# Kernel optimization log

Measured on AMD Instinct MI355X. Metric: run time of the kernel, lower is better.

The kernel has to match this reference:

```python
import jax, jax.numpy as jnp
import numpy as np

NUM_NODES = 100000
NUM_REL = 8
HIDDEN = 128
NUM_EDGES = 1600000
NUM_LAYERS = 2


def setup_inputs() -> dict:
    key = jax.random.key(0)
    k1, k2, k3, k4, k5 = jax.random.split(key, 5)
    x = jnp.arange(NUM_NODES, dtype=jnp.int64)
    edge_index = jax.random.randint(k1, (2, NUM_EDGES), 0, NUM_NODES, dtype=jnp.int64)
    edge_type = jax.random.randint(k2, (NUM_EDGES,), 0, NUM_REL, dtype=jnp.int64)
    emb = jax.random.normal(k3, (NUM_NODES, HIDDEN), dtype=jnp.float32) * 0.1
    W = jax.random.normal(k4, (NUM_LAYERS, NUM_REL, HIDDEN, HIDDEN), dtype=jnp.float32) * (1.0 / np.sqrt(HIDDEN))
    root = jax.random.normal(k5, (NUM_LAYERS, HIDDEN, HIDDEN), dtype=jnp.float32) * (1.0 / np.sqrt(HIDDEN))
    bias = jnp.zeros((NUM_LAYERS, HIDDEN), dtype=jnp.float32)
    return {"x": x, "edge_index": edge_index, "edge_type": edge_type,
            "emb": emb, "W": W, "root": root, "bias": bias}


def _rgcn_conv(h, src, dst, etype, W_l, root_l, bias_l):
    # h: [N, d]; W_l: [R, d, d]
    n = h.shape[0]
    r = W_l.shape[0]
    # Transform all nodes by every relation weight: [R, N, d]
    xW = jnp.einsum('nd,rdf->rnf', h, W_l)
    # Per-edge message gathered by (relation, source): [E, d]
    msg = xW[etype, src]
    # Mean-normalize per (target node, relation), matching PyG aggr='mean'
    seg = dst * r + etype  # combined (node, relation) segment id
    cnt = jax.ops.segment_sum(jnp.ones(msg.shape[0], dtype=h.dtype), seg,
                              num_segments=n * r)
    norm = 1.0 / jnp.maximum(cnt[seg], 1.0)
    agg = jax.ops.segment_sum(msg * norm[:, None], dst, num_segments=n)
    return agg + h @ root_l + bias_l


def reference(x, edge_index, edge_type, emb, W, root, bias):
    src, dst = edge_index[0], edge_index[1]
    h = emb[x]  # embedding lookup
    for l in range(NUM_LAYERS):
        h = _rgcn_conv(h, src, dst, edge_type, W[l], root[l], bias[l])
        h = jax.nn.relu(h)
    return h
```

## Files before the change

kernel.cpp:

```cpp
#include <hip/hip_runtime.h>

typedef unsigned int u32;
typedef unsigned short u16;
typedef __attribute__((ext_vector_type(8))) short short8;
typedef __attribute__((ext_vector_type(4))) float f32x4;

#define DD 128
#define RREL 8
#define NKT 9
#define SCAN_CHUNK 4096

static __device__ __forceinline__ u16 f2bf(float f) {
  u32 u = __builtin_bit_cast(u32, f);
  u32 r = (u + 0x7fffu + ((u >> 16) & 1u)) >> 16;
  return (u16)r;
}
static __device__ __forceinline__ float bflo(u32 v) { return __builtin_bit_cast(float, v << 16); }
static __device__ __forceinline__ float bfhi(u32 v) { return __builtin_bit_cast(float, v & 0xffff0000u); }

__global__ __launch_bounds__(256) void k_convw(const float* __restrict__ W,
                                               const float* __restrict__ root,
                                               uint4* __restrict__ wt) {
  int t = blockIdx.x * 256 + threadIdx.x;
  if (t >= 2 * NKT * 2048) return;
  int l = t / (NKT * 2048);
  int rem = t - l * (NKT * 2048);
  int kt = rem >> 11;
  int pos = rem & 2047;
  int col = pos >> 4;
  int cbx = pos & 15;
  int cb = cbx ^ (col & 7);
  int k0 = kt * DD + cb * 8;
  u16 vals[8];
#pragma unroll
  for (int i = 0; i < 8; ++i) {
    int k = k0 + i;
    float v;
    if (k < DD) {
      v = root[(size_t)l * DD * DD + k * DD + col];
    } else {
      int km = k - DD;
      v = W[((size_t)l * RREL + (km >> 7)) * DD * DD + (size_t)(km & 127) * DD + col];
    }
    vals[i] = f2bf(v);
  }
  wt[t] = *(uint4*)vals;
}

__global__ __launch_bounds__(256) void k_gather(const int* __restrict__ x,
                                                const float* __restrict__ emb,
                                                u16* __restrict__ h0, int N) {
  int t = blockIdx.x * 256 + threadIdx.x;
  if (t >= N * 16) return;
  int node = t >> 4, part = t & 15;
  const float4* e4 = (const float4*)(emb + (size_t)x[node] * DD + part * 8);
  float4 f0 = e4[0], f1 = e4[1];
  uint4 u;
  u.x = (u32)f2bf(f0.x) | ((u32)f2bf(f0.y) << 16);
  u.y = (u32)f2bf(f0.z) | ((u32)f2bf(f0.w) << 16);
  u.z = (u32)f2bf(f1.x) | ((u32)f2bf(f1.y) << 16);
  u.w = (u32)f2bf(f1.z) | ((u32)f2bf(f1.w) << 16);
  *(uint4*)(h0 + (size_t)node * DD + part * 8) = u;
}

__global__ __launch_bounds__(256) void k_hist(const int* __restrict__ ei,
                                              const int* __restrict__ et,
                                              int* __restrict__ cnt, int E) {
  int base = (blockIdx.x * 256 + threadIdx.x) * 4;
  if (base + 3 < E) {
    int4 d4 = *(const int4*)(ei + E + base);
    int4 t4 = *(const int4*)(et + base);
    atomicAdd(&cnt[d4.x * 8 + t4.x], 1);
    atomicAdd(&cnt[d4.y * 8 + t4.y], 1);
    atomicAdd(&cnt[d4.z * 8 + t4.z], 1);
    atomicAdd(&cnt[d4.w * 8 + t4.w], 1);
  } else {
    for (int e = base; e < E; ++e) atomicAdd(&cnt[ei[E + e] * 8 + et[e]], 1);
  }
}

__global__ __launch_bounds__(256) void k_scan_reduce(const int* __restrict__ cnt,
                                                     int* __restrict__ blksum, int nseg) {
  __shared__ int s[256];
  int b = blockIdx.x, t = threadIdx.x;
  int base = b * SCAN_CHUNK;
  int sum = 0;
  for (int i = 0; i < 16; ++i) {
    int idx = base + i * 256 + t;
    if (idx < nseg) sum += cnt[idx];
  }
  s[t] = sum;
  __syncthreads();
  for (int st = 128; st > 0; st >>= 1) {
    if (t < st) s[t] += s[t + st];
    __syncthreads();
  }
  if (t == 0) blksum[b] = s[0];
}

__global__ void k_scan_top(int* __restrict__ blksum, int nblk, int* __restrict__ off,
                           int nseg, int E) {
  if (threadIdx.x == 0 && blockIdx.x == 0) {
    int run = 0;
    for (int b = 0; b < nblk; ++b) { int v = blksum[b]; blksum[b] = run; run += v; }
    off[nseg] = E;
  }
}

__global__ __launch_bounds__(256) void k_scan_write(const int* __restrict__ cnt,
                                                    const int* __restrict__ blksum,
                                                    int* __restrict__ off, int nseg) {
  __shared__ int s[256];
  int b = blockIdx.x, t = threadIdx.x;
  int base = b * SCAN_CHUNK + t * 16;
  int v[16];
  int sum = 0;
#pragma unroll
  for (int i = 0; i < 16; ++i) {
    int idx = base + i;
    v[i] = (idx < nseg) ? cnt[idx] : 0;
    sum += v[i];
  }
  s[t] = sum;
  __syncthreads();
  for (int st = 1; st < 256; st <<= 1) {
    int add = (t >= st) ? s[t - st] : 0;
    __syncthreads();
    s[t] += add;
    __syncthreads();
  }
  int run = blksum[b] + s[t] - sum;
#pragma unroll
  for (int i = 0; i < 16; ++i) {
    int idx = base + i;
    if (idx < nseg) off[idx] = run;
    run += v[i];
  }
}

__global__ __launch_bounds__(256) void k_scatter(const int* __restrict__ ei,
                                                 const int* __restrict__ et,
                                                 int* __restrict__ fill,
                                                 int* __restrict__ sorted, int E) {
  int base = (blockIdx.x * 256 + threadIdx.x) * 4;
  if (base + 3 < E) {
    int4 s4 = *(const int4*)(ei + base);
    int4 d4 = *(const int4*)(ei + E + base);
    int4 t4 = *(const int4*)(et + base);
    int p0 = atomicAdd(&fill[d4.x * 8 + t4.x], 1);
    int p1 = atomicAdd(&fill[d4.y * 8 + t4.y], 1);
    int p2 = atomicAdd(&fill[d4.z * 8 + t4.z], 1);
    int p3 = atomicAdd(&fill[d4.w * 8 + t4.w], 1);
    sorted[p0] = s4.x;
    sorted[p1] = s4.y;
    sorted[p2] = s4.z;
    sorted[p3] = s4.w;
  } else {
    for (int e = base; e < E; ++e) {
      int pos = atomicAdd(&fill[ei[E + e] * 8 + et[e]], 1);
      sorted[pos] = ei[e];
    }
  }
}

static __device__ __forceinline__ void add8(float* a, uint4 v) {
  a[0] += bflo(v.x); a[1] += bfhi(v.x);
  a[2] += bflo(v.y); a[3] += bfhi(v.y);
  a[4] += bflo(v.z); a[5] += bfhi(v.z);
  a[6] += bflo(v.w); a[7] += bfhi(v.w);
}

template <bool LAST>
__global__ __launch_bounds__(512, 4) void k_fused(const u16* __restrict__ hin,
                                                  const int* __restrict__ off,
                                                  const int* __restrict__ sorted,
                                                  const uint4* __restrict__ wt,
                                                  const float* __restrict__ bias,
                                                  u16* __restrict__ hout,
                                                  float* __restrict__ dout, int M) {
  __shared__ uint4 ldsB[2][2048];
  int tid = threadIdx.x, wave = tid >> 6, lane = tid & 63;
  int p = lane & 15, q = lane >> 4;
  int row = blockIdx.x * 128 + wave * 16 + p;
  int arc = row < M ? row : M - 1;
  f32x4 acc[8];
#pragma unroll
  for (int c = 0; c < 8; ++c) acc[c] = (f32x4)0.f;

#define STAGE(KT, BUF)                                                                   \
  do {                                                                                   \
    const uint4* gsrc = wt + (size_t)(KT) * 2048;                                        \
    _Pragma("unroll") for (int i_ = 0; i_ < 4; ++i_) {                                   \
      int cid_ = i_ * 512 + tid;                                                         \
      __builtin_amdgcn_global_load_lds(                                                  \
          (const __attribute__((address_space(1))) uint4*)(gsrc + cid_),                 \
          (__attribute__((address_space(3))) uint4*)&ldsB[BUF][cid_], 16, 0, 0);         \
    }                                                                                    \
  } while (0)

  STAGE(0, 0);
  for (int kt = 0; kt < NKT; ++kt) {
    short8 afrag[4];
    if (kt == 0) {
      const short8* ap = (const short8*)(hin + (size_t)arc * DD) + q;
#pragma unroll
      for (int kc = 0; kc < 4; ++kc) afrag[kc] = ap[kc * 4];
    } else {
      int r = kt - 1;
      int s = 0, e = 0;
      if (row < M) {
        int sb = row * 8 + r;
        s = off[sb];
        e = off[sb + 1];
      }
      float a[32];
#pragma unroll
      for (int i = 0; i < 32; ++i) a[i] = 0.f;
      for (int j = s; j < e; ++j) {
        int src = sorted[j];
        const uint4* hp = (const uint4*)(hin + (size_t)src * DD) + q;
        uint4 v0 = hp[0], v1 = hp[4], v2 = hp[8], v3 = hp[12];
        add8(a + 0, v0);
        add8(a + 8, v1);
        add8(a + 16, v2);
        add8(a + 24, v3);
      }
      float norm = (e > s) ? 1.0f / (float)(e - s) : 0.f;
      u16 fr[32];
#pragma unroll
      for (int i = 0; i < 32; ++i) fr[i] = f2bf(a[i] * norm);
#pragma unroll
      for (int kc = 0; kc < 4; ++kc) afrag[kc] = *(const short8*)(fr + kc * 8);
    }
    int cur = kt & 1;
    __syncthreads();
    if (kt + 1 < NKT) STAGE(kt + 1, cur ^ 1);
#pragma unroll
    for (int kc = 0; kc < 4; ++kc) {
      int chunk = kc * 4 + q;
#pragma unroll
      for (int c = 0; c < 8; ++c) {
        int col = c * 16 + p;
        const short8* bp = (const short8*)&ldsB[cur][col * 16 + (chunk ^ (col & 7))];
        acc[c] = __builtin_amdgcn_mfma_f32_16x16x32_bf16(afrag[kc], *bp, acc[c], 0, 0, 0);
      }
    }
  }
#undef STAGE

  int crow0 = blockIdx.x * 128 + wave * 16 + (q << 2);
#pragma unroll
  for (int c = 0; c < 8; ++c) {
    int col = c * 16 + p;
    float bv = bias[col];
#pragma unroll
    for (int i = 0; i < 4; ++i) {
      int rw = crow0 + i;
      if (rw < M) {
        float v = fmaxf(acc[c][i] + bv, 0.f);
        if (LAST) dout[(size_t)rw * DD + col] = v;
        else hout[(size_t)rw * DD + col] = f2bf(v);
      }
    }
  }
}

extern "C" void kernel_launch(void* const* d_in, const int* in_sizes, int n_in,
                              void* d_out, int out_size, void* d_ws, size_t ws_size,
                              hipStream_t stream) {
  const int* x = (const int*)d_in[0];
  const int* ei = (const int*)d_in[1];
  const int* et = (const int*)d_in[2];
  const float* emb = (const float*)d_in[3];
  const float* W = (const float*)d_in[4];
  const float* root = (const float*)d_in[5];
  const float* bias = (const float*)d_in[6];

  const int N = in_sizes[0];
  const int E = in_sizes[2];
  const int NSEG = N * RREL;

  size_t o = 0;
  auto al = [&](size_t b) { size_t r = o; o = (o + b + 255) & ~(size_t)255; return r; };
  size_t off_o = al(((size_t)NSEG + 1) * 4);
  size_t cnt_o = al((size_t)NSEG * 4);
  size_t fill_o = al((size_t)NSEG * 4);
  size_t sorted_o = al((size_t)E * 4);
  size_t blk_o = al(4096);
  size_t wt_o = al((size_t)2 * NKT * 2048 * 16);
  size_t h0_o = al((size_t)N * DD * 2);
  size_t h1_o = al((size_t)N * DD * 2);
  (void)h1_o;

  char* ws = (char*)d_ws;
  int* off = (int*)(ws + off_o);
  int* cnt = (int*)(ws + cnt_o);
  int* fill = (int*)(ws + fill_o);
  int* sorted = (int*)(ws + sorted_o);
  int* blks = (int*)(ws + blk_o);
  uint4* wt = (uint4*)(ws + wt_o);
  u16* h0 = (u16*)(ws + h0_o);
  u16* h1 = (u16*)(ws + h1_o);
  float* outf = (float*)d_out;

  k_convw<<<(2 * NKT * 2048 + 255) / 256, 256, 0, stream>>>(W, root, wt);
  k_gather<<<(N * 16 + 255) / 256, 256, 0, stream>>>(x, emb, h0, N);
  hipMemsetAsync(cnt, 0, (size_t)NSEG * 4, stream);
  int egrid = ((E + 3) / 4 + 255) / 256;
  k_hist<<<egrid, 256, 0, stream>>>(ei, et, cnt, E);
  int nblk = (NSEG + SCAN_CHUNK - 1) / SCAN_CHUNK;
  k_scan_reduce<<<nblk, 256, 0, stream>>>(cnt, blks, NSEG);
  k_scan_top<<<1, 64, 0, stream>>>(blks, nblk, off, NSEG, E);
  k_scan_write<<<nblk, 256, 0, stream>>>(cnt, blks, off, NSEG);
  hipMemcpyAsync(fill, off, (size_t)NSEG * 4, hipMemcpyDeviceToDevice, stream);
  k_scatter<<<egrid, 256, 0, stream>>>(ei, et, fill, sorted, E);

  int gx = (N + 127) / 128;
  k_fused<false><<<gx, 512, 0, stream>>>(h0, off, sorted, wt, bias, h1, nullptr, N);
  k_fused<true><<<gx, 512, 0, stream>>>(h1, off, sorted, wt + (size_t)NKT * 2048,
                                        bias + DD, nullptr, outf, N);
}
```

Baseline: 547.3 us.

## Gather all relation aggregates up front, then run MFMA loop without sync stalls

```diff
diff --git a/kernel.cpp b/kernel.cpp
--- a/kernel.cpp
+++ b/kernel.cpp
@@ -171,7 +171,7 @@
 }
 
 template <bool LAST>
-__global__ __launch_bounds__(512, 4) void k_fused(const u16* __restrict__ hin,
+__global__ __launch_bounds__(512, 2) void k_fused(const u16* __restrict__ hin,
                                                   const int* __restrict__ off,
                                                   const int* __restrict__ sorted,
                                                   const uint4* __restrict__ wt,
@@ -183,9 +183,6 @@
   int p = lane & 15, q = lane >> 4;
   int row = blockIdx.x * 128 + wave * 16 + p;
   int arc = row < M ? row : M - 1;
-  f32x4 acc[8];
-#pragma unroll
-  for (int c = 0; c < 8; ++c) acc[c] = (f32x4)0.f;
 
 #define STAGE(KT, BUF)                                                                   \
   do {                                                                                   \
@@ -199,39 +196,52 @@
   } while (0)
 
   STAGE(0, 0);
+
+  short8 afr[NKT][4];
+  {
+    const short8* ap = (const short8*)(hin + (size_t)arc * DD) + q;
+#pragma unroll
+    for (int kc = 0; kc < 4; ++kc) afr[0][kc] = ap[kc * 4];
+  }
+  int row8 = arc * 8;
+  int4 oA = *(const int4*)(off + row8);
+  int4 oB = *(const int4*)(off + row8 + 4);
+  int oC = off[row8 + 8];
+  int ov[9] = {oA.x, oA.y, oA.z, oA.w, oB.x, oB.y, oB.z, oB.w, oC};
+#pragma unroll
+  for (int r = 0; r < RREL; ++r) {
+    int s = ov[r], e = ov[r + 1];
+    float a[32];
+#pragma unroll
+    for (int i = 0; i < 32; ++i) a[i] = 0.f;
+    int j = s;
+    for (; j + 2 <= e; j += 2) {
+      int s0 = sorted[j], s1 = sorted[j + 1];
+      const uint4* h0p = (const uint4*)(hin + (size_t)s0 * DD) + q;
+      const uint4* h1p = (const uint4*)(hin + (size_t)s1 * DD) + q;
+      uint4 u0 = h0p[0], u1 = h0p[4], u2 = h0p[8], u3 = h0p[12];
+      uint4 w0 = h1p[0], w1 = h1p[4], w2 = h1p[8], w3 = h1p[12];
+      add8(a + 0, u0);  add8(a + 8, u1);  add8(a + 16, u2);  add8(a + 24, u3);
+      add8(a + 0, w0);  add8(a + 8, w1);  add8(a + 16, w2);  add8(a + 24, w3);
+    }
+    if (j < e) {
+      const uint4* h0p = (const uint4*)(hin + (size_t)sorted[j] * DD) + q;
+      uint4 u0 = h0p[0], u1 = h0p[4], u2 = h0p[8], u3 = h0p[12];
+      add8(a + 0, u0);  add8(a + 8, u1);  add8(a + 16, u2);  add8(a + 24, u3);
+    }
+    float norm = (e > s) ? 1.0f / (float)(e - s) : 0.f;
+    u16 fr[32];
+#pragma unroll
+    for (int i = 0; i < 32; ++i) fr[i] = f2bf(a[i] * norm);
+#pragma unroll
+    for (int kc = 0; kc < 4; ++kc) afr[r + 1][kc] = *(const short8*)(fr + kc * 8);
+  }
+
+  f32x4 acc[8];
+#pragma unroll
+  for (int c = 0; c < 8; ++c) acc[c] = (f32x4)0.f;
+#pragma unroll
   for (int kt = 0; kt < NKT; ++kt) {
-    short8 afrag[4];
-    if (kt == 0) {
-      const short8* ap = (const short8*)(hin + (size_t)arc * DD) + q;
-#pragma unroll
-      for (int kc = 0; kc < 4; ++kc) afrag[kc] = ap[kc * 4];
-    } else {
-      int r = kt - 1;
-      int s = 0, e = 0;
-      if (row < M) {
-        int sb = row * 8 + r;
-        s = off[sb];
-        e = off[sb + 1];
-      }
-      float a[32];
-#pragma unroll
-      for (int i = 0; i < 32; ++i) a[i] = 0.f;
-      for (int j = s; j < e; ++j) {
-        int src = sorted[j];
-        const uint4* hp = (const uint4*)(hin + (size_t)src * DD) + q;
-        uint4 v0 = hp[0], v1 = hp[4], v2 = hp[8], v3 = hp[12];
-        add8(a + 0, v0);
-        add8(a + 8, v1);
-        add8(a + 16, v2);
-        add8(a + 24, v3);
-      }
-      float norm = (e > s) ? 1.0f / (float)(e - s) : 0.f;
-      u16 fr[32];
-#pragma unroll
-      for (int i = 0; i < 32; ++i) fr[i] = f2bf(a[i] * norm);
-#pragma unroll
-      for (int kc = 0; kc < 4; ++kc) afrag[kc] = *(const short8*)(fr + kc * 8);
-    }
     int cur = kt & 1;
     __syncthreads();
     if (kt + 1 < NKT) STAGE(kt + 1, cur ^ 1);
@@ -242,7 +252,7 @@
       for (int c = 0; c < 8; ++c) {
         int col = c * 16 + p;
         const short8* bp = (const short8*)&ldsB[cur][col * 16 + (chunk ^ (col & 7))];
-        acc[c] = __builtin_amdgcn_mfma_f32_16x16x32_bf16(afrag[kc], *bp, acc[c], 0, 0, 0);
+        acc[c] = __builtin_amdgcn_mfma_f32_16x16x32_bf16(afr[kt][kc], *bp, acc[c], 0, 0, 0);
       }
     }
   }
```

Measured after the change: 815.4 us. 1.49x slower.
